# Kernel optimization log

Measured on AMD Instinct MI355X. Metric: run time of the kernel, lower is better.

Reference implementation:

```python
import jax, jax.numpy as jnp
import numpy as np

N = 50000        # num nodes
E = 800000       # num edges (before self loops)
IN = 256         # in_channels
H = 4            # heads
C = 32           # out_channels per head
NEG_SLOPE = 0.2


def _glorot(key, shape):
    fan = shape[-2] * (shape[-1] if len(shape) > 2 else 1) + shape[-1]
    # PyG glorot: uniform(-s, s) with s = sqrt(6 / (fan_in + fan_out))
    s = float(np.sqrt(6.0 / (shape[-2] + shape[-1])))
    return jax.random.uniform(key, shape, jnp.float32, -s, s)


def setup_inputs() -> dict:
    key = jax.random.key(0)
    k1, k2, k3, k4, k5 = jax.random.split(key, 5)
    x = jax.random.normal(k1, (N, IN), jnp.float32)
    src = jax.random.randint(k2, (E,), 0, N)
    dst = jax.random.randint(k3, (E,), 0, N)
    # guarantee no self loops (module removes them then re-adds exactly N loops)
    dst = jnp.where(dst == src, (dst + 1) % N, dst)
    edge_index = jnp.stack([src, dst]).astype(jnp.int32)
    weight = _glorot(k4, (IN, H * C))
    att = _glorot(k5, (1, H, 2 * C))
    bias = jnp.zeros((H * C,), jnp.float32)
    return {"x": x, "weight": weight, "att": att, "bias": bias,
            "edge_index": edge_index}


def reference(x, weight, att, bias, edge_index):
    n = x.shape[0]
    # linear projection -> [N, H, C]
    h = (x @ weight).reshape(n, H, C)
    # add self loops (input edge_index has none)
    loops = jnp.arange(n, dtype=edge_index.dtype)
    ei = jnp.concatenate([edge_index, jnp.stack([loops, loops])], axis=1)
    src, dst = ei[0], ei[1]          # flow source_to_target: j=src(row 0), i=dst(row 1)
    x_j = h[src]                     # [E', H, C] source features
    x_i = h[dst]                     # [E', H, C] target features
    wl = att[:, :, :C]               # applied to x_i (first half of concat)
    wr = att[:, :, C:]               # applied to x_j
    alpha = (x_i * wl).sum(-1) + (x_j * wr).sum(-1)   # [E', H]
    alpha = jax.nn.leaky_relu(alpha, NEG_SLOPE)
    # NOTE: module normalizes softmax over edge_index[0] (src) segments
    seg = src
    amax = jax.ops.segment_max(alpha, seg, num_segments=n)
    alpha = jnp.exp(alpha - amax[seg])
    denom = jax.ops.segment_sum(alpha, seg, num_segments=n)
    alpha = alpha / (denom[seg] + 1e-16)
    # weighted messages, aggregated at edge_index[i] = edge_index[1] (dst)
    msg = x_j * alpha[:, :, None]                     # [E', H, C]
    out = jax.ops.segment_sum(msg, dst, num_segments=n)  # [N, H, C]
    return out.reshape(n, H * C) + bias
```

## Files before the change

kernel.cpp:

```cpp
#include <hip/hip_runtime.h>
#include <hip/hip_fp16.h>
#include <math.h>


#define NH 4
#define CH 32
#define HC 128
#define IND 256
#define NEG_SLOPE 0.2f
#define CSH 8
#define NCB_MAX 256
#define CHUNK 4096
#define BCAP 6144

typedef __attribute__((ext_vector_type(8))) short bf16x8;
typedef __attribute__((ext_vector_type(16))) float f32x16;

__device__ __forceinline__ unsigned short f2bf(float f) {
    unsigned int u = __float_as_uint(f);
    unsigned int r = (u + 0x7FFFu + ((u >> 16) & 1u)) >> 16;
    return (unsigned short)r;
}
__device__ __forceinline__ float bf2f(unsigned short s) {
    return __uint_as_float(((unsigned int)s) << 16);
}

__global__ __launch_bounds__(256) void k_wprep(const float* __restrict__ W,
                                               unsigned short* __restrict__ WT_bf,
                                               int* __restrict__ gcurS,
                                               int* __restrict__ gcurD) {
    int t = blockIdx.x * 256 + threadIdx.x;
    if (blockIdx.x == 0) { gcurS[threadIdx.x] = 0; gcurD[threadIdx.x] = 0; }
    if (t < IND * HC) {
        int c = t >> 8;
        int k = t & 255;
        WT_bf[t] = f2bf(W[k * HC + c]);
    }
}

__global__ __launch_bounds__(256) void k_gemm_mfma(const float* __restrict__ x,
                                                   const unsigned short* __restrict__ WT_bf,
                                                   const float* __restrict__ att,
                                                   unsigned short* __restrict__ h_bf,
                                                   float* __restrict__ al,
                                                   float* __restrict__ ar, int N) {
    __shared__ float cs[128 * 129];
    unsigned short* wsT = (unsigned short*)cs;

    const int tid  = threadIdx.x;
    const int row0 = blockIdx.x * 128;
    const int wave = tid >> 6;
    const int lane = tid & 63;
    const int n32  = lane & 31;
    const int half = lane >> 5;

    {
        int c  = tid >> 1;
        int kh = (tid & 1) * 128;
        const unsigned short* src = WT_bf + c * IND + kh;
        unsigned short* dst = wsT + c * 258 + kh;
#pragma unroll
        for (int j = 0; j < 128; j += 8)
            *(int4*)(dst + j) = *(const int4*)(src + j);
    }
    __syncthreads();

    const int row   = row0 + wave * 32 + n32;
    const bool valid = row < N;
    const float* xrow = x + (size_t)row * IND + half * 8;

    f32x16 acc[4];
#pragma unroll
    for (int t = 0; t < 4; t++)
#pragma unroll
        for (int r = 0; r < 16; r++) acc[t][r] = 0.0f;

#pragma unroll 4
    for (int s = 0; s < 16; s++) {
        float4 v0 = make_float4(0.f, 0.f, 0.f, 0.f);
        float4 v1 = v0;
        if (valid) {
            v0 = *(const float4*)(xrow + s * 16);
            v1 = *(const float4*)(xrow + s * 16 + 4);
        }
        bf16x8 a;
        a[0] = (short)f2bf(v0.x); a[1] = (short)f2bf(v0.y);
        a[2] = (short)f2bf(v0.z); a[3] = (short)f2bf(v0.w);
        a[4] = (short)f2bf(v1.x); a[5] = (short)f2bf(v1.y);
        a[6] = (short)f2bf(v1.z); a[7] = (short)f2bf(v1.w);
#pragma unroll
        for (int t = 0; t < 4; t++) {
            bf16x8 b = *(const bf16x8*)(wsT + (t * 32 + n32) * 258 + s * 16 + half * 8);
            acc[t] = __builtin_amdgcn_mfma_f32_32x32x16_bf16(a, b, acc[t], 0, 0, 0);
        }
    }
    __syncthreads();

#pragma unroll
    for (int t = 0; t < 4; t++)
#pragma unroll
        for (int r = 0; r < 16; r++) {
            int rl = wave * 32 + (r & 3) + 8 * (r >> 2) + 4 * half;
            cs[rl * 129 + t * 32 + n32] = acc[t][r];
        }
    __syncthreads();

    const int rl   = tid >> 1;
    const int chf  = tid & 1;
    const int orow = row0 + rl;
    if (orow < N) {
        const float* cr = cs + rl * 129 + chf * 64;
        unsigned short* hp = h_bf + (size_t)orow * HC + chf * 64;
#pragma unroll
        for (int c = 0; c < 64; c += 8) {
            ushort4 o0, o1;
            o0.x = f2bf(cr[c]);     o0.y = f2bf(cr[c + 1]);
            o0.z = f2bf(cr[c + 2]); o0.w = f2bf(cr[c + 3]);
            o1.x = f2bf(cr[c + 4]); o1.y = f2bf(cr[c + 5]);
            o1.z = f2bf(cr[c + 6]); o1.w = f2bf(cr[c + 7]);
            *(ushort4*)(hp + c) = o0;
            *(ushort4*)(hp + c + 4) = o1;
        }
        const int h0 = 2 * chf, h1 = 2 * chf + 1;
        const float* w0 = att + h0 * (2 * CH);
        const float* w1 = att + h1 * (2 * CH);
        float sl0 = 0.f, sr0 = 0.f, sl1 = 0.f, sr1 = 0.f;
#pragma unroll
        for (int c = 0; c < CH; c++) {
            float v0 = cr[c];
            float v1 = cr[CH + c];
            sl0 += v0 * w0[c];  sr0 += v0 * w0[CH + c];
            sl1 += v1 * w1[c];  sr1 += v1 * w1[CH + c];
        }
        al[orow * NH + h0] = sl0;  al[orow * NH + h1] = sl1;
        ar[orow * NH + h0] = sr0;  ar[orow * NH + h1] = sr1;
    }
}

__global__ __launch_bounds__(256) void k_scatterC(const int* __restrict__ ei,
                                                  int* __restrict__ gcurS,
                                                  int* __restrict__ gcurD,
                                                  unsigned int* __restrict__ recS,
                                                  unsigned int* __restrict__ recD,
                                                  int E, int NE, int ncb) {
    __shared__ unsigned int srt[CHUNK];
    __shared__ int cnt[NCB_MAX], off[NCB_MAX], cur[NCB_MAX], gpos[NCB_MAX], sc[256];
    const int tid = threadIdx.x;
    const int t0  = blockIdx.x * CHUNK;
    const int m   = min(CHUNK, NE - t0);

    unsigned int myrec[CHUNK / 256];
    int nmy = 0;
    for (int i = tid; i < m; i += 256) {
        int t = t0 + i;
        int src, dst;
        if (t < E) { src = ei[t]; dst = ei[E + t]; }
        else       { src = dst = t - E; }
        myrec[nmy++] = (unsigned int)src | ((unsigned int)dst << 16);
    }

    for (int side = 0; side < 2; side++) {
        cnt[tid] = 0;
        __syncthreads();
        int mybkt[CHUNK / 256];
        for (int k = 0; k < nmy; k++) {
            unsigned int r = myrec[k];
            int node = side ? (int)(r >> 16) : (int)(r & 0xFFFFu);
            mybkt[k] = node >> CSH;
            atomicAdd(&cnt[mybkt[k]], 1);
        }
        __syncthreads();
        int v = cnt[tid];
        sc[tid] = v;
        __syncthreads();
        for (int o = 1; o < 256; o <<= 1) {
            int t = (tid >= o) ? sc[tid - o] : 0;
            __syncthreads();
            sc[tid] += t;
            __syncthreads();
        }
        off[tid] = sc[tid] - v;
        cur[tid] = sc[tid] - v;
        __syncthreads();
        for (int k = 0; k < nmy; k++) {
            int p = atomicAdd(&cur[mybkt[k]], 1);
            srt[p] = myrec[k];
        }
        __syncthreads();
        int* gcur = side ? gcurD : gcurS;
        if (tid < ncb) {
            int c = cnt[tid];
            gpos[tid] = c ? atomicAdd(&gcur[tid], c) : 0;
        }
        __syncthreads();
        unsigned int* recX = side ? recD : recS;
        for (int i = tid; i < m; i += 256) {
            unsigned int r = srt[i];
            int node = side ? (int)(r >> 16) : (int)(r & 0xFFFFu);
            int cb = node >> CSH;
            int p  = gpos[cb] + (i - off[cb]);
            if (p < BCAP)
                recX[(size_t)cb * BCAP + p] = r;
        }
        __syncthreads();
    }
}

__global__ __launch_bounds__(256) void k_bucket(const unsigned int* __restrict__ recS,
                                                const unsigned int* __restrict__ recD,
                                                const int* __restrict__ gcurS,
                                                const int* __restrict__ gcurD,
                                                const float* __restrict__ al,
                                                const float* __restrict__ ar,
                                                unsigned short* __restrict__ adjD,
                                                int* __restrict__ rowB,
                                                int* __restrict__ rowE,
                                                float* __restrict__ arw,
                                                int ncb, int N) {
    __shared__ int cnt[256], cur[256], sc[256];
    __shared__ float lsums[256 * NH];
    __shared__ float lar[256 * NH];
    const int tid = threadIdx.x;

    if (blockIdx.x < ncb) {
        const int cb = blockIdx.x;
        const int b0 = cb * BCAP;
        const int tot_rec = min(gcurD[cb], BCAP);

        cnt[tid] = 0;
        __syncthreads();
        for (int i = tid; i < tot_rec; i += 256) {
            unsigned int r = recD[b0 + i];
            atomicAdd(&cnt[(r >> 16) & 255], 1);
        }
        __syncthreads();
        int v = cnt[tid];
        sc[tid] = v;
        __syncthreads();
        for (int o = 1; o < 256; o <<= 1) {
            int t = (tid >= o) ? sc[tid - o] : 0;
            __syncthreads();
            sc[tid] += t;
            __syncthreads();
        }
        int ex = sc[tid] - v;
        int node_g = (cb << CSH) + tid;
        if (node_g < N) { rowB[node_g] = b0 + ex; rowE[node_g] = b0 + ex + v; }
        cur[tid] = ex;
        __syncthreads();
        for (int i = tid; i < tot_rec; i += 256) {
            unsigned int r = recD[b0 + i];
            int node = (int)(r >> 16) & 255;
            int p = atomicAdd(&cur[node], 1);
            adjD[b0 + p] = (unsigned short)(r & 0xFFFFu);
        }
    } else {
        const int cb = blockIdx.x - ncb;
        const int b0 = cb * BCAP;
        const int b1 = b0 + min(gcurS[cb], BCAP);
        const int node_g = (cb << CSH) + tid;

        float4 arv = make_float4(0.f, 0.f, 0.f, 0.f);
        if (node_g < N) arv = *(const float4*)(ar + (size_t)node_g * NH);
        *(float4*)(lar + tid * NH) = arv;
        *(float4*)(lsums + tid * NH) = make_float4(0.f, 0.f, 0.f, 0.f);
        __syncthreads();

        for (int i = b0 + tid; i < b1; i += 256) {
            unsigned int r = recS[i];
            int slot = (int)(r & 255u);
            int dst  = (int)(r >> 16);
            float4 alv = *(const float4*)(al + (size_t)dst * NH);
            const float* av = lar + slot * NH;
            float a0 = alv.x + av[0], a1 = alv.y + av[1];
            float a2 = alv.z + av[2], a3 = alv.w + av[3];
            a0 = (a0 > 0.f) ? a0 : NEG_SLOPE * a0;
            a1 = (a1 > 0.f) ? a1 : NEG_SLOPE * a1;
            a2 = (a2 > 0.f) ? a2 : NEG_SLOPE * a2;
            a3 = (a3 > 0.f) ? a3 : NEG_SLOPE * a3;
            float* sp = lsums + slot * NH;
            atomicAdd(sp + 0, __expf(a0));
            atomicAdd(sp + 1, __expf(a1));
            atomicAdd(sp + 2, __expf(a2));
            atomicAdd(sp + 3, __expf(a3));
        }
        __syncthreads();

        if (node_g < N) {
            const float* sp = lsums + tid * NH;
            float4 p0 = make_float4(arv.x, 1.0f / (sp[0] + 1e-16f),
                                    arv.y, 1.0f / (sp[1] + 1e-16f));
            float4 p1 = make_float4(arv.z, 1.0f / (sp[2] + 1e-16f),
                                    arv.w, 1.0f / (sp[3] + 1e-16f));
            *(float4*)(arw + (size_t)node_g * 8)     = p0;
            *(float4*)(arw + (size_t)node_g * 8 + 4) = p1;
        }
    }
}

__global__ __launch_bounds__(256) void k_agg(const int* __restrict__ rowB,
                                             const int* __restrict__ rowE,
                                             const unsigned short* __restrict__ adjD,
                                             const float* __restrict__ al,
                                             const float* __restrict__ arw,
                                             const unsigned short* __restrict__ h_bf,
                                             const float* __restrict__ bias,
                                             float* __restrict__ out, int N) {
    const int g = threadIdx.x >> 5;
    const int n = blockIdx.x * 8 + g;
    if (n >= N) return;
    const int l  = threadIdx.x & 31;
    const int c0 = l * 4;
    const int hh = l >> 3;
    const int beg = rowB[n], end = rowE[n];
    const float alv = al[n * NH + hh];

    float a0 = 0.f, a1 = 0.f, a2 = 0.f, a3 = 0.f;

    for (int base = beg; base < end; base += 32) {
        int idx = base + l;
        int av  = (idx < end) ? (int)adjD[idx] : 0;
        int cnt = min(32, end - base);
        int e = 0;
        for (; e + 4 <= cnt; e += 4) {
            int s0 = __shfl(av, e,     32);
            int s1 = __shfl(av, e + 1, 32);
            int s2 = __shfl(av, e + 2, 32);
            int s3 = __shfl(av, e + 3, 32);
            ushort4 u0 = *(const ushort4*)(h_bf + (size_t)s0 * HC + c0);
            ushort4 u1 = *(const ushort4*)(h_bf + (size_t)s1 * HC + c0);
            ushort4 u2 = *(const ushort4*)(h_bf + (size_t)s2 * HC + c0);
            ushort4 u3 = *(const ushort4*)(h_bf + (size_t)s3 * HC + c0);
            float2 p0 = *(const float2*)(arw + (size_t)s0 * 8 + hh * 2);
            float2 p1 = *(const float2*)(arw + (size_t)s1 * 8 + hh * 2);
            float2 p2 = *(const float2*)(arw + (size_t)s2 * 8 + hh * 2);
            float2 p3 = *(const float2*)(arw + (size_t)s3 * 8 + hh * 2);
            float t0 = alv + p0.x; t0 = (t0 > 0.f) ? t0 : NEG_SLOPE * t0;
            float t1 = alv + p1.x; t1 = (t1 > 0.f) ? t1 : NEG_SLOPE * t1;
            float t2 = alv + p2.x; t2 = (t2 > 0.f) ? t2 : NEG_SLOPE * t2;
            float t3 = alv + p3.x; t3 = (t3 > 0.f) ? t3 : NEG_SLOPE * t3;
            float w0 = __expf(t0) * p0.y;
            float w1 = __expf(t1) * p1.y;
            float w2 = __expf(t2) * p2.y;
            float w3 = __expf(t3) * p3.y;
            a0 += bf2f(u0.x) * w0; a1 += bf2f(u0.y) * w0;
            a2 += bf2f(u0.z) * w0; a3 += bf2f(u0.w) * w0;
            a0 += bf2f(u1.x) * w1; a1 += bf2f(u1.y) * w1;
            a2 += bf2f(u1.z) * w1; a3 += bf2f(u1.w) * w1;
            a0 += bf2f(u2.x) * w2; a1 += bf2f(u2.y) * w2;
            a2 += bf2f(u2.z) * w2; a3 += bf2f(u2.w) * w2;
            a0 += bf2f(u3.x) * w3; a1 += bf2f(u3.y) * w3;
            a2 += bf2f(u3.z) * w3; a3 += bf2f(u3.w) * w3;
        }
        for (; e < cnt; e++) {
            int s0 = __shfl(av, e, 32);
            ushort4 u0 = *(const ushort4*)(h_bf + (size_t)s0 * HC + c0);
            float2 p0 = *(const float2*)(arw + (size_t)s0 * 8 + hh * 2);
            float t0 = alv + p0.x; t0 = (t0 > 0.f) ? t0 : NEG_SLOPE * t0;
            float w0 = __expf(t0) * p0.y;
            a0 += bf2f(u0.x) * w0; a1 += bf2f(u0.y) * w0;
            a2 += bf2f(u0.z) * w0; a3 += bf2f(u0.w) * w0;
        }
    }
    float4 b4 = *(const float4*)(bias + c0);
    *(float4*)(out + (size_t)n * HC + c0) =
        make_float4(a0 + b4.x, a1 + b4.y, a2 + b4.z, a3 + b4.w);
}

extern "C" void kernel_launch(void* const* d_in, const int* in_sizes, int n_in,
                              void* d_out, int out_size, void* d_ws, size_t ws_size,
                              hipStream_t stream) {
    const float* x    = (const float*)d_in[0];
    const float* W    = (const float*)d_in[1];
    const float* att  = (const float*)d_in[2];
    const float* bias = (const float*)d_in[3];
    const int*   ei   = (const int*)d_in[4];

    const int N  = in_sizes[0] / IND;
    const int E  = in_sizes[4] / 2;
    const int NE = E + N;
    const int ncb = (N + (1 << CSH) - 1) >> CSH;
    float* out = (float*)d_out;
    const int nodeTot = N * NH;
    const size_t capTot = (size_t)ncb * BCAP;

    unsigned short* h_bf  = (unsigned short*)d_ws;
    unsigned short* WT_bf = h_bf + (size_t)N * HC;
    float* al   = (float*)(WT_bf + IND * HC);
    float* ar   = al + nodeTot;
    float* arw  = ar + nodeTot;
    unsigned int* recS = (unsigned int*)(arw + (size_t)N * 8);
    unsigned int* recD = recS + capTot;
    unsigned short* adjD = (unsigned short*)(recD + capTot);
    int* rowB    = (int*)(adjD + capTot + (capTot & 1));
    int* rowE    = rowB + N;
    int* gcurS   = rowE + N;
    int* gcurD   = gcurS + NCB_MAX;

    k_wprep<<<(IND * HC + 255) / 256, 256, 0, stream>>>(W, WT_bf, gcurS, gcurD);
    k_gemm_mfma<<<(N + 127) / 128, 256, 0, stream>>>(x, WT_bf, att, h_bf, al, ar, N);
    k_scatterC<<<(NE + CHUNK - 1) / CHUNK, 256, 0, stream>>>(ei, gcurS, gcurD,
                                                             recS, recD, E, NE, ncb);
    k_bucket<<<2 * ncb, 256, 0, stream>>>(recS, recD, gcurS, gcurD, al, ar,
                                          adjD, rowB, rowE, arw, ncb, N);
    k_agg<<<(N + 7) / 8, 256, 0, stream>>>(rowB, rowE, adjD, al, arw, h_bf,
                                           bias, out, N);
}
```

Baseline: 213.3 us.

## Merge edge scatter into GEMM kernel and unroll softmax-denominator loop by two

The edge bucketing scatter and the MFMA projection GEMM are independent, so they now run as two block ranges of a single launch: the first nsb blocks do the scatter and the rest do the GEMM. This removes one kernel launch and the serialization between the two stages so they can overlap on the GPU. The scatter reuses the GEMM's large shared buffer, which raises its shared-memory footprint and can lower occupancy for scatter blocks. Separately, the denominator accumulation loop in k_bucket is unrolled by two to overlap independent gathers of al.

```diff
diff --git a/kernel.cpp b/kernel.cpp
--- a/kernel.cpp
+++ b/kernel.cpp
@@ -38,17 +38,94 @@
     }
 }
 
-__global__ __launch_bounds__(256) void k_gemm_mfma(const float* __restrict__ x,
-                                                   const unsigned short* __restrict__ WT_bf,
-                                                   const float* __restrict__ att,
-                                                   unsigned short* __restrict__ h_bf,
-                                                   float* __restrict__ al,
-                                                   float* __restrict__ ar, int N) {
+__global__ __launch_bounds__(256) void k_gs(const float* __restrict__ x,
+                                            const unsigned short* __restrict__ WT_bf,
+                                            const float* __restrict__ att,
+                                            unsigned short* __restrict__ h_bf,
+                                            float* __restrict__ al,
+                                            float* __restrict__ ar,
+                                            const int* __restrict__ ei,
+                                            int* __restrict__ gcurS,
+                                            int* __restrict__ gcurD,
+                                            unsigned int* __restrict__ recS,
+                                            unsigned int* __restrict__ recD,
+                                            int E, int NE, int ncb, int nsb, int N) {
     __shared__ float cs[128 * 129];
+
+    const int tid = threadIdx.x;
+
+    if (blockIdx.x < nsb) {
+        unsigned int* srt = (unsigned int*)cs;
+        int* cnt  = (int*)(srt + CHUNK);
+        int* off  = cnt + NCB_MAX;
+        int* cur  = off + NCB_MAX;
+        int* gpos = cur + NCB_MAX;
+        int* sc   = gpos + NCB_MAX;
+
+        const int t0 = blockIdx.x * CHUNK;
+        const int m  = min(CHUNK, NE - t0);
+
+        unsigned int myrec[CHUNK / 256];
+        int nmy = 0;
+        for (int i = tid; i < m; i += 256) {
+            int t = t0 + i;
+            int src, dst;
+            if (t < E) { src = ei[t]; dst = ei[E + t]; }
+            else       { src = dst = t - E; }
+            myrec[nmy++] = (unsigned int)src | ((unsigned int)dst << 16);
+        }
+
+        for (int side = 0; side < 2; side++) {
+            cnt[tid] = 0;
+            __syncthreads();
+            int mybkt[CHUNK / 256];
+            for (int k = 0; k < nmy; k++) {
+                unsigned int r = myrec[k];
+                int node = side ? (int)(r >> 16) : (int)(r & 0xFFFFu);
+                mybkt[k] = node >> CSH;
+                atomicAdd(&cnt[mybkt[k]], 1);
+            }
+            __syncthreads();
+            int v = cnt[tid];
+            sc[tid] = v;
+            __syncthreads();
+            for (int o = 1; o < 256; o <<= 1) {
+                int t = (tid >= o) ? sc[tid - o] : 0;
+                __syncthreads();
+                sc[tid] += t;
+                __syncthreads();
+            }
+            off[tid] = sc[tid] - v;
+            cur[tid] = sc[tid] - v;
+            __syncthreads();
+            for (int k = 0; k < nmy; k++) {
+                int p = atomicAdd(&cur[mybkt[k]], 1);
+                srt[p] = myrec[k];
+            }
+            __syncthreads();
+            int* gcur = side ? gcurD : gcurS;
+            if (tid < ncb) {
+                int c = cnt[tid];
+                gpos[tid] = c ? atomicAdd(&gcur[tid], c) : 0;
+            }
+            __syncthreads();
+            unsigned int* recX = side ? recD : recS;
+            for (int i = tid; i < m; i += 256) {
+                unsigned int r = srt[i];
+                int node = side ? (int)(r >> 16) : (int)(r & 0xFFFFu);
+                int cb = node >> CSH;
+                int p  = gpos[cb] + (i - off[cb]);
+                if (p < BCAP)
+                    recX[(size_t)cb * BCAP + p] = r;
+            }
+            __syncthreads();
+        }
+        return;
+    }
+
     unsigned short* wsT = (unsigned short*)cs;
 
-    const int tid  = threadIdx.x;
-    const int row0 = blockIdx.x * 128;
+    const int row0 = (blockIdx.x - nsb) * 128;
     const int wave = tid >> 6;
     const int lane = tid & 63;
     const int n32  = lane & 31;
@@ -134,75 +211,6 @@
         }
         al[orow * NH + h0] = sl0;  al[orow * NH + h1] = sl1;
         ar[orow * NH + h0] = sr0;  ar[orow * NH + h1] = sr1;
-    }
-}
-
-__global__ __launch_bounds__(256) void k_scatterC(const int* __restrict__ ei,
-                                                  int* __restrict__ gcurS,
-                                                  int* __restrict__ gcurD,
-                                                  unsigned int* __restrict__ recS,
-                                                  unsigned int* __restrict__ recD,
-                                                  int E, int NE, int ncb) {
-    __shared__ unsigned int srt[CHUNK];
-    __shared__ int cnt[NCB_MAX], off[NCB_MAX], cur[NCB_MAX], gpos[NCB_MAX], sc[256];
-    const int tid = threadIdx.x;
-    const int t0  = blockIdx.x * CHUNK;
-    const int m   = min(CHUNK, NE - t0);
-
-    unsigned int myrec[CHUNK / 256];
-    int nmy = 0;
-    for (int i = tid; i < m; i += 256) {
-        int t = t0 + i;
-        int src, dst;
-        if (t < E) { src = ei[t]; dst = ei[E + t]; }
-        else       { src = dst = t - E; }
-        myrec[nmy++] = (unsigned int)src | ((unsigned int)dst << 16);
-    }
-
-    for (int side = 0; side < 2; side++) {
-        cnt[tid] = 0;
-        __syncthreads();
-        int mybkt[CHUNK / 256];
-        for (int k = 0; k < nmy; k++) {
-            unsigned int r = myrec[k];
-            int node = side ? (int)(r >> 16) : (int)(r & 0xFFFFu);
-            mybkt[k] = node >> CSH;
-            atomicAdd(&cnt[mybkt[k]], 1);
-        }
-        __syncthreads();
-        int v = cnt[tid];
-        sc[tid] = v;
-        __syncthreads();
-        for (int o = 1; o < 256; o <<= 1) {
-            int t = (tid >= o) ? sc[tid - o] : 0;
-            __syncthreads();
-            sc[tid] += t;
-            __syncthreads();
-        }
-        off[tid] = sc[tid] - v;
-        cur[tid] = sc[tid] - v;
-        __syncthreads();
-        for (int k = 0; k < nmy; k++) {
-            int p = atomicAdd(&cur[mybkt[k]], 1);
-            srt[p] = myrec[k];
-        }
-        __syncthreads();
-        int* gcur = side ? gcurD : gcurS;
-        if (tid < ncb) {
-            int c = cnt[tid];
-            gpos[tid] = c ? atomicAdd(&gcur[tid], c) : 0;
-        }
-        __syncthreads();
-        unsigned int* recX = side ? recD : recS;
-        for (int i = tid; i < m; i += 256) {
-            unsigned int r = srt[i];
-            int node = side ? (int)(r >> 16) : (int)(r & 0xFFFFu);
-            int cb = node >> CSH;
-            int p  = gpos[cb] + (i - off[cb]);
-            if (p < BCAP)
-                recX[(size_t)cb * BCAP + p] = r;
-        }
-        __syncthreads();
     }
 }
 
@@ -266,7 +274,40 @@
         *(float4*)(lsums + tid * NH) = make_float4(0.f, 0.f, 0.f, 0.f);
         __syncthreads();
 
-        for (int i = b0 + tid; i < b1; i += 256) {
+        int i = b0 + tid;
+        for (; i + 256 < b1; i += 512) {
+            unsigned int r0 = recS[i];
+            unsigned int r1 = recS[i + 256];
+            int sl0 = (int)(r0 & 255u), dst0 = (int)(r0 >> 16);
+            int sl1 = (int)(r1 & 255u), dst1 = (int)(r1 >> 16);
+            float4 av0 = *(const float4*)(al + (size_t)dst0 * NH);
+            float4 av1 = *(const float4*)(al + (size_t)dst1 * NH);
+            const float* w0 = lar + sl0 * NH;
+            const float* w1 = lar + sl1 * NH;
+            float a0 = av0.x + w0[0], a1 = av0.y + w0[1];
+            float a2 = av0.z + w0[2], a3 = av0.w + w0[3];
+            float c0 = av1.x + w1[0], c1 = av1.y + w1[1];
+            float c2 = av1.z + w1[2], c3 = av1.w + w1[3];
+            a0 = (a0 > 0.f) ? a0 : NEG_SLOPE * a0;
+            a1 = (a1 > 0.f) ? a1 : NEG_SLOPE * a1;
+            a2 = (a2 > 0.f) ? a2 : NEG_SLOPE * a2;
+            a3 = (a3 > 0.f) ? a3 : NEG_SLOPE * a3;
+            c0 = (c0 > 0.f) ? c0 : NEG_SLOPE * c0;
+            c1 = (c1 > 0.f) ? c1 : NEG_SLOPE * c1;
+            c2 = (c2 > 0.f) ? c2 : NEG_SLOPE * c2;
+            c3 = (c3 > 0.f) ? c3 : NEG_SLOPE * c3;
+            float* s0 = lsums + sl0 * NH;
+            float* s1 = lsums + sl1 * NH;
+            atomicAdd(s0 + 0, __expf(a0));
+            atomicAdd(s0 + 1, __expf(a1));
+            atomicAdd(s0 + 2, __expf(a2));
+            atomicAdd(s0 + 3, __expf(a3));
+            atomicAdd(s1 + 0, __expf(c0));
+            atomicAdd(s1 + 1, __expf(c1));
+            atomicAdd(s1 + 2, __expf(c2));
+            atomicAdd(s1 + 3, __expf(c3));
+        }
+        if (i < b1) {
             unsigned int r = recS[i];
             int slot = (int)(r & 255u);
             int dst  = (int)(r >> 16);
@@ -380,6 +421,8 @@
     const int E  = in_sizes[4] / 2;
     const int NE = E + N;
     const int ncb = (N + (1 << CSH) - 1) >> CSH;
+    const int nsb = (NE + CHUNK - 1) / CHUNK;
+    const int ngb = (N + 127) / 128;
     float* out = (float*)d_out;
     const int nodeTot = N * NH;
     const size_t capTot = (size_t)ncb * BCAP;
@@ -398,9 +441,9 @@
     int* gcurD   = gcurS + NCB_MAX;
 
     k_wprep<<<(IND * HC + 255) / 256, 256, 0, stream>>>(W, WT_bf, gcurS, gcurD);
-    k_gemm_mfma<<<(N + 127) / 128, 256, 0, stream>>>(x, WT_bf, att, h_bf, al, ar, N);
-    k_scatterC<<<(NE + CHUNK - 1) / CHUNK, 256, 0, stream>>>(ei, gcurS, gcurD,
-                                                             recS, recD, E, NE, ncb);
+    k_gs<<<nsb + ngb, 256, 0, stream>>>(x, WT_bf, att, h_bf, al, ar, ei,
+                                        gcurS, gcurD, recS, recD,
+                                        E, NE, ncb, nsb, N);
     k_bucket<<<2 * ncb, 256, 0, stream>>>(recS, recD, gcurS, gcurD, al, ar,
                                           adjD, rowB, rowE, arw, ncb, N);
     k_agg<<<(N + 7) / 8, 256, 0, stream>>>(rowB, rowE, adjD, al, arw, h_bf,
```

Result: faster. 206.9 us (-3.0%).
